# Kernel optimization log

Hardware: AMD Instinct MI355X
Metric: run time of the kernel (lower is better)

## Reference

```python
import jax, jax.numpy as jnp
import numpy as np

H = 256          # decoder_size
MAX_LENGTH = 64
VOCAB = 3


def _cell(x, h, c, w_ih, w_hh, b_ih, b_hh):
    # PyTorch LSTM cell, gate order i, f, g, o
    g = x @ w_ih.T + h @ w_hh.T + b_ih + b_hh
    i, f, gg, o = jnp.split(g, 4, axis=-1)
    c = jax.nn.sigmoid(f) * c + jax.nn.sigmoid(i) * jnp.tanh(gg)
    h = jax.nn.sigmoid(o) * jnp.tanh(c)
    return h, c


def _final_state(xs, w_ih, w_hh, b_ih, b_hh):
    # run a unidirectional LSTM over xs [T,B,D], return final (h, c)
    B = xs.shape[1]
    h0 = jnp.zeros((B, H), xs.dtype)
    c0 = jnp.zeros((B, H), xs.dtype)
    def step(carry, x):
        h, c = _cell(x, carry[0], carry[1], w_ih, w_hh, b_ih, b_hh)
        return (h, c), None
    (h, c), _ = jax.lax.scan(step, (h0, c0), xs)
    return h, c


def setup_inputs() -> dict:
    key = jax.random.key(0)
    ks = jax.random.split(key, 20)
    T, B, D = 512, 128, 1024
    s = jnp.float32(0.05)  # keep gates out of saturation
    def p(k, shape):
        return jax.random.normal(k, shape, jnp.float32) * s
    return {
        "x": jax.random.normal(ks[0], (T, B, D), jnp.float32),
        "ew_ih_f": p(ks[1], (4 * H, D)), "ew_hh_f": p(ks[2], (4 * H, H)),
        "eb_ih_f": p(ks[3], (4 * H,)),   "eb_hh_f": p(ks[4], (4 * H,)),
        "ew_ih_b": p(ks[5], (4 * H, D)), "ew_hh_b": p(ks[6], (4 * H, H)),
        "eb_ih_b": p(ks[7], (4 * H,)),   "eb_hh_b": p(ks[8], (4 * H,)),
        "dw_ih0": p(ks[9], (4 * H, H)),  "dw_hh0": p(ks[10], (4 * H, H)),
        "db_ih0": p(ks[11], (4 * H,)),   "db_hh0": p(ks[12], (4 * H,)),
        "dw_ih1": p(ks[13], (4 * H, H)), "dw_hh1": p(ks[14], (4 * H, H)),
        "db_ih1": p(ks[15], (4 * H,)),   "db_hh1": p(ks[16], (4 * H,)),
        "lw": p(ks[17], (VOCAB, H)),     "lb": p(ks[18], (VOCAB,)),
    }


def reference(x, ew_ih_f, ew_hh_f, eb_ih_f, eb_hh_f,
              ew_ih_b, ew_hh_b, eb_ih_b, eb_hh_b,
              dw_ih0, dw_hh0, db_ih0, db_hh0,
              dw_ih1, dw_hh1, db_ih1, db_hh1,
              lw, lb):
    # --- bidirectional encoder: only final hidden states are used ---
    hf, cf = _final_state(x, ew_ih_f, ew_hh_f, eb_ih_f, eb_hh_f)          # forward dir
    hb, cb = _final_state(x[::-1], ew_ih_b, ew_hh_b, eb_ih_b, eb_hh_b)    # backward dir
    # encoder h_n/c_n stacked as [fwd, bwd] -> decoder layer0, layer1 init
    B = x.shape[1]
    inp0 = jnp.zeros((B, H), x.dtype)
    def step(carry, _):
        inp, h0, c0, h1, c1 = carry
        h0, c0 = _cell(inp, h0, c0, dw_ih0, dw_hh0, db_ih0, db_hh0)
        h1, c1 = _cell(h0, h1, c1, dw_ih1, dw_hh1, db_ih1, db_hh1)
        out = h1 @ lw.T + lb  # [B, VOCAB]
        return (h1, h0, c0, h1, c1), out
    _, outs = jax.lax.scan(step, (inp0, hf, cf, hb, cb), None, length=MAX_LENGTH)
    return outs  # [MAX_LENGTH, B, VOCAB]
```

## Files before the change

### kernel.cpp

```cpp
#include <hip/hip_runtime.h>
#include <hip/hip_bf16.h>
#include <math.h>


typedef unsigned short u16;
typedef unsigned int u32;
typedef unsigned long long u64;
typedef _Float16 f16;
typedef f16 f16x8 __attribute__((ext_vector_type(8)));
typedef u16 u16x8 __attribute__((ext_vector_type(8)));
typedef u32 u32x4 __attribute__((ext_vector_type(4)));
typedef float f32x4 __attribute__((ext_vector_type(4)));

__device__ __forceinline__ u16 f2h(float f) {
  return __builtin_bit_cast(unsigned short, (f16)f);
}
__device__ __forceinline__ float h2f(u16 h) {
  return (float)__builtin_bit_cast(f16, h);
}
__device__ __forceinline__ u32 packf16(float a, float b) {
  return (u32)f2h(a) | ((u32)f2h(b) << 16);
}
__device__ __forceinline__ u64 ald64(const u64* p) {
  return __hip_atomic_load(p, __ATOMIC_RELAXED, __HIP_MEMORY_SCOPE_AGENT);
}
__device__ __forceinline__ void ast64(u64* p, u64 v) {
  __hip_atomic_store(p, v, __ATOMIC_RELAXED, __HIP_MEMORY_SCOPE_AGENT);
}

#define SENT 0xFFFFFFFFFFFFFFFFull

__global__ __launch_bounds__(256) void init_k(u32* hglob, u32* r0, u32* r1) {
  int gid = blockIdx.x * 256 + threadIdx.x;
  if (gid < 131072)       hglob[gid] = 0xFFFFFFFFu;
  else if (gid < 196608)  r0[gid - 131072] = 0xFFFFFFFFu;
  else                    r1[gid - 196608] = 0xFFFFFFFFu;
}

__global__ __launch_bounds__(256) void convert_k(
    const float* __restrict__ x,
    const float* __restrict__ wfm, const float* __restrict__ wbm,
    const float* __restrict__ bif, const float* __restrict__ bhf,
    const float* __restrict__ bib, const float* __restrict__ bhb,
    const float* __restrict__ dbi0, const float* __restrict__ dbh0,
    const float* __restrict__ dbi1, const float* __restrict__ dbh1,
    u16* __restrict__ xh, u16* __restrict__ wh,
    float* __restrict__ bias2, float* __restrict__ dbias) {
  const long NX = 67108864L, NW = 1048576L;
  long gid = (long)blockIdx.x * 256 + threadIdx.x;
  if (gid < 1024) {
    bias2[gid]        = bif[gid] + bhf[gid];
    bias2[1024 + gid] = bib[gid] + bhb[gid];
    dbias[gid]        = dbi0[gid] + dbh0[gid];
    dbias[1024 + gid] = dbi1[gid] + dbh1[gid];
  }
  long total4 = (NX + 2 * NW) >> 2;
  long stride = (long)gridDim.x * 256;
  for (long q = gid; q < total4; q += stride) {
    long i = q << 2;
    const float* src; u16* dst; long o;
    if (i < NX)            { src = x;   dst = xh;      o = i; }
    else if (i < NX + NW)  { src = wfm; dst = wh;      o = i - NX; }
    else                   { src = wbm; dst = wh + NW; o = i - NX - NW; }
    float4 v = *(const float4*)&src[o];
    dst[o + 0] = f2h(v.x); dst[o + 1] = f2h(v.y);
    dst[o + 2] = f2h(v.z); dst[o + 3] = f2h(v.w);
  }
}

__global__ __launch_bounds__(256) void convert_we3_k(
    const float* __restrict__ whf, const float* __restrict__ whb,
    u16* __restrict__ wenc3) {
  int o = blockIdx.x * 256 + threadIdx.x;
  int j = o & 7, lane = (o >> 3) & 63, ks = (o >> 9) & 7;
  int w = (o >> 12) & 3, cg = (o >> 14) & 15, d = o >> 18;
  int ri = lane & 15;
  int gcol = (ri & 3) * 256 + cg * 16 + w * 4 + (ri >> 2);
  int k = ks * 32 + (lane >> 4) * 8 + j;
  const float* wsrc = d ? whb : whf;
  wenc3[o] = f2h(wsrc[gcol * 256 + k]);
}

__global__ __launch_bounds__(256) void convert_wdec_k(
    const float* __restrict__ wi0, const float* __restrict__ wh0,
    const float* __restrict__ wi1, const float* __restrict__ wh1,
    u16* __restrict__ wdec) {
  int o = blockIdx.x * 256 + threadIdx.x;
  int j = o & 7, lane = (o >> 3) & 63, ks = (o >> 9) & 15;
  int w = (o >> 13) & 3, cg = (o >> 15) & 15, L = o >> 19;
  int ri = lane & 15;
  int row = (ri & 3) * 256 + cg * 16 + w * 4 + (ri >> 2);
  int k = ks * 32 + (lane >> 4) * 8 + j;
  const float* wi = L ? wi1 : wi0;
  const float* wh = L ? wh1 : wh0;
  float v = (k < 256) ? wi[row * 256 + k] : wh[row * 256 + k - 256];
  wdec[o] = f2h(v);
}

__global__ __launch_bounds__(256) void xproj_gemm(
    const u16* __restrict__ xh, const u16* __restrict__ wh,
    const float* __restrict__ bias2, float* __restrict__ xp) {
  __shared__ u16 Al[128][40];
  __shared__ u16 Bl[128][40];
  int bid = blockIdx.x;
  int dir = bid >> 12, rem = bid & 4095, tb = rem >> 3, nb = rem & 7;
  int tsrc = dir ? (511 - tb) : tb;
  const u16* A  = xh + (long)tsrc * (128 * 1024);
  const u16* Bw = wh + (long)dir * (1024 * 1024) + (long)nb * (128 * 1024);
  float* C = xp + ((long)(dir * 512 + tb) * 128) * 1024 + nb * 128;
  const float* bias = bias2 + dir * 1024 + nb * 128;

  int tid = threadIdx.x, lane = tid & 63, wid = tid >> 6;
  int wr = wid >> 1, wc = wid & 1;
  int srow = tid >> 1, scol = (tid & 1) * 16;
  int fr = lane & 15, ko = lane >> 4;

  f32x4 acc[4][4] = {};
  for (int k0 = 0; k0 < 1024; k0 += 32) {
    u16x8 a0 = *(const u16x8*)&A[(long)srow * 1024 + k0 + scol];
    u16x8 a1 = *(const u16x8*)&A[(long)srow * 1024 + k0 + scol + 8];
    u16x8 b0 = *(const u16x8*)&Bw[(long)srow * 1024 + k0 + scol];
    u16x8 b1 = *(const u16x8*)&Bw[(long)srow * 1024 + k0 + scol + 8];
    __syncthreads();
    *(u16x8*)&Al[srow][scol]     = a0;
    *(u16x8*)&Al[srow][scol + 8] = a1;
    *(u16x8*)&Bl[srow][scol]     = b0;
    *(u16x8*)&Bl[srow][scol + 8] = b1;
    __syncthreads();
    f16x8 af[4], bf[4];
#pragma unroll
    for (int i = 0; i < 4; ++i)
      af[i] = __builtin_bit_cast(f16x8, *(const u16x8*)&Al[wr * 64 + i * 16 + fr][ko * 8]);
#pragma unroll
    for (int jf = 0; jf < 4; ++jf)
      bf[jf] = __builtin_bit_cast(f16x8, *(const u16x8*)&Bl[wc * 64 + jf * 16 + fr][ko * 8]);
#pragma unroll
    for (int i = 0; i < 4; ++i)
#pragma unroll
      for (int jf = 0; jf < 4; ++jf)
        acc[i][jf] = __builtin_amdgcn_mfma_f32_16x16x32_f16(af[i], bf[jf], acc[i][jf], 0, 0, 0);
  }
  int fq = lane >> 4;
#pragma unroll
  for (int i = 0; i < 4; ++i)
#pragma unroll
    for (int jf = 0; jf < 4; ++jf) {
      int col = wc * 64 + jf * 16 + fr;
      float bv = bias[col];
#pragma unroll
      for (int e = 0; e < 4; ++e) {
        int row = wr * 64 + i * 16 + fq * 4 + e;
        C[(long)row * 1024 + col] = acc[i][jf][e] + bv;
      }
    }
}

__global__ __launch_bounds__(256, 1) void encoder_k(
    const u16* __restrict__ wenc3, const float* __restrict__ xp,
    u32* hglob,
    float* h0b, float* h1b, float* cfb, float* cbb) {
  int b = blockIdx.x;
  int g16 = ((b >> 7) << 3) | (b & 7);
  int cg = (b >> 3) & 15;
  int d = g16 >> 3, bg = g16 & 7;
  int tid = threadIdx.x, lane = tid & 63, w = tid >> 6;
  int brow = lane & 15, lq = lane >> 4;
  int hswz = (brow & 7) << 4;

  __shared__ __align__(16) char hlds[2][8192];
  __shared__ __align__(16) u16 hstage[16][16];

  f16x8 wfr[8];
  {
    const u16* wb = wenc3 + (((long)d * 16 + cg) * 4 + w) * 4096 + lane * 8;
#pragma unroll
    for (int ks = 0; ks < 8; ++ks)
      wfr[ks] = __builtin_bit_cast(f16x8, *(const u16x8*)(wb + (long)ks * 512));
  }

  float c_state = 0.f;
  long xpbase = ((long)(d * 512) * 128 + bg * 16 + brow) * 1024 + cg * 16 + w * 4 + lq;
  float xpv[4];
#pragma unroll
  for (int g = 0; g < 4; ++g) xpv[g] = xp[xpbase + g * 256];

  u64* hg = (u64*)hglob;
  long ringbase = (long)g16 * 4096;
  int gcg = tid >> 4, gbrow = tid & 15;
  int gldsbase = gbrow * 512 + gcg * 32;
  int gswz = (gbrow & 7) << 4;
  __syncthreads();

  for (int t = 0; t < 512; ++t) {
    if (t != 0) {
      const long gb = ringbase + (long)(t & 3) * 1024 + 4 * tid;
      u64 v0 = SENT, v1 = SENT, v2 = SENT, v3 = SENT;
      for (;;) {
        bool ok = true;
        if (v0 == SENT) { v0 = ald64(hg + gb + 0); ok &= (v0 != SENT); }
        if (v1 == SENT) { v1 = ald64(hg + gb + 1); ok &= (v1 != SENT); }
        if (v2 == SENT) { v2 = ald64(hg + gb + 2); ok &= (v2 != SENT); }
        if (v3 == SENT) { v3 = ald64(hg + gb + 3); ok &= (v3 != SENT); }
        if (ok) break;
      }
      if (tid < 64)
        ast64(hg + ringbase + (long)((t + 2) & 3) * 1024 + cg * 64 + tid, SENT);
      char* hwr = hlds[t & 1];
      *(u32x4*)(hwr + (gldsbase ^ gswz)) =
          (u32x4){ (u32)v0, (u32)(v0 >> 32), (u32)v1, (u32)(v1 >> 32) };
      *(u32x4*)(hwr + ((gldsbase + 16) ^ gswz)) =
          (u32x4){ (u32)v2, (u32)(v2 >> 32), (u32)v3, (u32)(v3 >> 32) };
    }
    __syncthreads();

    f32x4 acc0 = {}, acc1 = {};
    if (t != 0) {
      const char* hrd = hlds[t & 1];
#pragma unroll
      for (int ks = 0; ks < 8; ++ks) {
        f16x8 hf = *(const f16x8*)(hrd + ((brow * 512 + ks * 64 + lq * 16) ^ hswz));
        if (ks & 1) acc1 = __builtin_amdgcn_mfma_f32_16x16x32_f16(wfr[ks], hf, acc1, 0, 0, 0);
        else        acc0 = __builtin_amdgcn_mfma_f32_16x16x32_f16(wfr[ks], hf, acc0, 0, 0, 0);
      }
    }

    float iv = 1.f / (1.f + expf(-(acc0[0] + acc1[0] + xpv[0])));
    float fv = 1.f / (1.f + expf(-(acc0[1] + acc1[1] + xpv[1])));
    float gg = tanhf(acc0[2] + acc1[2] + xpv[2]);
    float ov = 1.f / (1.f + expf(-(acc0[3] + acc1[3] + xpv[3])));
    c_state = fv * c_state + iv * gg;
    float hval = ov * tanhf(c_state);

    if (t < 511) {
      hstage[brow][w * 4 + lq] = f2h(hval);
      __syncthreads();
      asm volatile("s_waitcnt vmcnt(0)" ::: "memory");
      if (tid < 64) {
        u64 v = *(const u64*)&hstage[tid >> 2][(tid & 3) * 4];
        ast64(hg + ringbase + (long)((t + 1) & 3) * 1024 + cg * 64 + tid, v);
      }
      long xb2 = xpbase + (long)(t + 1) * 131072;
#pragma unroll
      for (int g = 0; g < 4; ++g) xpv[g] = xp[xb2 + g * 256];
    } else {
      int rowg = bg * 16 + brow, colg = cg * 16 + w * 4 + lq;
      (d ? h1b : h0b)[32768 + rowg * 256 + colg] = hval;
      (d ? cbb : cfb)[rowg * 256 + colg] = c_state;
    }
  }
}

__global__ __launch_bounds__(256, 1) void decoder_k(
    const u16* __restrict__ wdec, const float* __restrict__ dbias,
    const float* __restrict__ h0b, const float* __restrict__ h1b,
    const float* __restrict__ cfb, const float* __restrict__ cbb,
    u32* r0, u32* r1, float* __restrict__ hist) {
  int b = blockIdx.x;
  int bg = b & 7, cg = b >> 3;
  int tid = threadIdx.x, lane = tid & 63, w = tid >> 6;
  int brow = lane & 15, lq = lane >> 4;
  int hswz = (brow & 7) << 4;
  int col = cg * 16 + w * 4 + lq;

  __shared__ __align__(16) char hA[8192];
  __shared__ __align__(16) char hB[8192];
  __shared__ __align__(16) u16 hstage[16][16];

  f16x8 w0[16], w1[16];
  {
    const u16* p0 = wdec + ((long)(cg * 4 + w)) * 8192 + lane * 8;
    const u16* p1 = wdec + ((long)((16 + cg) * 4 + w)) * 8192 + lane * 8;
#pragma unroll
    for (int ks = 0; ks < 16; ++ks) {
      w0[ks] = __builtin_bit_cast(f16x8, *(const u16x8*)(p0 + (long)ks * 512));
      w1[ks] = __builtin_bit_cast(f16x8, *(const u16x8*)(p1 + (long)ks * 512));
    }
  }
  float b0[4], b1[4];
#pragma unroll
  for (int g = 0; g < 4; ++g) {
    b0[g] = dbias[g * 256 + col];
    b1[g] = dbias[1024 + g * 256 + col];
  }
  float c0 = cfb[(bg * 16 + brow) * 256 + col];
  float c1 = cbb[(bg * 16 + brow) * 256 + col];

  int gbrow = tid & 15, gcg = tid >> 4;
  int gldsbase = gbrow * 512 + gcg * 32;
  int gswz = (gbrow & 7) << 4;
  {
    const float* sA = h0b + 32768 + (bg * 16 + gbrow) * 256 + gcg * 16;
    const float* sB = h1b + 32768 + (bg * 16 + gbrow) * 256 + gcg * 16;
    u32 wa[8], wb[8];
#pragma unroll
    for (int i = 0; i < 8; ++i) {
      wa[i] = packf16(sA[2 * i], sA[2 * i + 1]);
      wb[i] = packf16(sB[2 * i], sB[2 * i + 1]);
    }
    *(u32x4*)(hA + (gldsbase ^ gswz))        = (u32x4){wa[0], wa[1], wa[2], wa[3]};
    *(u32x4*)(hA + ((gldsbase + 16) ^ gswz)) = (u32x4){wa[4], wa[5], wa[6], wa[7]};
    *(u32x4*)(hB + (gldsbase ^ gswz))        = (u32x4){wb[0], wb[1], wb[2], wb[3]};
    *(u32x4*)(hB + ((gldsbase + 16) ^ gswz)) = (u32x4){wb[4], wb[5], wb[6], wb[7]};
  }
  __syncthreads();

  u64* g0 = (u64*)r0;
  u64* g1 = (u64*)r1;
  long ring = (long)bg * 4096;

  for (int t = 0; t < 64; ++t) {
    f32x4 a0 = {}, a1 = {};
    if (t > 0) {
#pragma unroll
      for (int ks = 0; ks < 8; ++ks) {
        f16x8 hf = *(const f16x8*)(hB + ((brow * 512 + ks * 64 + lq * 16) ^ hswz));
        if (ks & 1) a1 = __builtin_amdgcn_mfma_f32_16x16x32_f16(w0[ks], hf, a1, 0, 0, 0);
        else        a0 = __builtin_amdgcn_mfma_f32_16x16x32_f16(w0[ks], hf, a0, 0, 0, 0);
      }
    }
#pragma unroll
    for (int ks = 0; ks < 8; ++ks) {
      f16x8 hf = *(const f16x8*)(hA + ((brow * 512 + ks * 64 + lq * 16) ^ hswz));
      if (ks & 1) a1 = __builtin_amdgcn_mfma_f32_16x16x32_f16(w0[8 + ks], hf, a1, 0, 0, 0);
      else        a0 = __builtin_amdgcn_mfma_f32_16x16x32_f16(w0[8 + ks], hf, a0, 0, 0, 0);
    }
    {
      float iv = 1.f / (1.f + expf(-(a0[0] + a1[0] + b0[0])));
      float fv = 1.f / (1.f + expf(-(a0[1] + a1[1] + b0[1])));
      float gg = tanhf(a0[2] + a1[2] + b0[2]);
      float ov = 1.f / (1.f + expf(-(a0[3] + a1[3] + b0[3])));
      c0 = fv * c0 + iv * gg;
      float h0v = ov * tanhf(c0);
      hstage[brow][w * 4 + lq] = f2h(h0v);
    }
    __syncthreads();
    if (tid < 64)
      ast64(g0 + ring + (long)((t + 2) & 3) * 1024 + cg * 64 + tid, SENT);
    asm volatile("s_waitcnt vmcnt(0)" ::: "memory");
    if (tid < 64) {
      u64 v = *(const u64*)&hstage[tid >> 2][(tid & 3) * 4];
      ast64(g0 + ring + (long)(t & 3) * 1024 + cg * 64 + tid, v);
    }
    {
      const long gb = ring + (long)(t & 3) * 1024 + 4 * tid;
      u64 v0 = SENT, v1 = SENT, v2 = SENT, v3 = SENT;
      for (;;) {
        bool ok = true;
        if (v0 == SENT) { v0 = ald64(g0 + gb + 0); ok &= (v0 != SENT); }
        if (v1 == SENT) { v1 = ald64(g0 + gb + 1); ok &= (v1 != SENT); }
        if (v2 == SENT) { v2 = ald64(g0 + gb + 2); ok &= (v2 != SENT); }
        if (v3 == SENT) { v3 = ald64(g0 + gb + 3); ok &= (v3 != SENT); }
        if (ok) break;
      }
      *(u32x4*)(hA + (gldsbase ^ gswz)) =
          (u32x4){ (u32)v0, (u32)(v0 >> 32), (u32)v1, (u32)(v1 >> 32) };
      *(u32x4*)(hA + ((gldsbase + 16) ^ gswz)) =
          (u32x4){ (u32)v2, (u32)(v2 >> 32), (u32)v3, (u32)(v3 >> 32) };
    }
    __syncthreads();

    a0 = (f32x4){}; a1 = (f32x4){};
#pragma unroll
    for (int ks = 0; ks < 8; ++ks) {
      f16x8 hf = *(const f16x8*)(hA + ((brow * 512 + ks * 64 + lq * 16) ^ hswz));
      if (ks & 1) a1 = __builtin_amdgcn_mfma_f32_16x16x32_f16(w1[ks], hf, a1, 0, 0, 0);
      else        a0 = __builtin_amdgcn_mfma_f32_16x16x32_f16(w1[ks], hf, a0, 0, 0, 0);
    }
#pragma unroll
    for (int ks = 0; ks < 8; ++ks) {
      f16x8 hf = *(const f16x8*)(hB + ((brow * 512 + ks * 64 + lq * 16) ^ hswz));
      if (ks & 1) a1 = __builtin_amdgcn_mfma_f32_16x16x32_f16(w1[8 + ks], hf, a1, 0, 0, 0);
      else        a0 = __builtin_amdgcn_mfma_f32_16x16x32_f16(w1[8 + ks], hf, a0, 0, 0, 0);
    }
    {
      float iv = 1.f / (1.f + expf(-(a0[0] + a1[0] + b1[0])));
      float fv = 1.f / (1.f + expf(-(a0[1] + a1[1] + b1[1])));
      float gg = tanhf(a0[2] + a1[2] + b1[2]);
      float ov = 1.f / (1.f + expf(-(a0[3] + a1[3] + b1[3])));
      c1 = fv * c1 + iv * gg;
      float h1v = ov * tanhf(c1);
      hstage[brow][w * 4 + lq] = f2h(h1v);
    }
    __syncthreads();
    if (tid < 64) {
      u64 v = *(const u64*)&hstage[tid >> 2][(tid & 3) * 4];
      float4 hv4 = { h2f((u16)v), h2f((u16)(v >> 16)),
                     h2f((u16)(v >> 32)), h2f((u16)(v >> 48)) };
      *(float4*)&hist[((long)t * 128 + bg * 16 + (tid >> 2)) * 256 + cg * 16 + (tid & 3) * 4] = hv4;
    }
    if (t < 63) {
      if (tid < 64)
        ast64(g1 + ring + (long)((t + 2) & 3) * 1024 + cg * 64 + tid, SENT);
      asm volatile("s_waitcnt vmcnt(0)" ::: "memory");
      if (tid < 64) {
        u64 v = *(const u64*)&hstage[tid >> 2][(tid & 3) * 4];
        ast64(g1 + ring + (long)(t & 3) * 1024 + cg * 64 + tid, v);
      }
      const long gb = ring + (long)(t & 3) * 1024 + 4 * tid;
      u64 v0 = SENT, v1 = SENT, v2 = SENT, v3 = SENT;
      for (;;) {
        bool ok = true;
        if (v0 == SENT) { v0 = ald64(g1 + gb + 0); ok &= (v0 != SENT); }
        if (v1 == SENT) { v1 = ald64(g1 + gb + 1); ok &= (v1 != SENT); }
        if (v2 == SENT) { v2 = ald64(g1 + gb + 2); ok &= (v2 != SENT); }
        if (v3 == SENT) { v3 = ald64(g1 + gb + 3); ok &= (v3 != SENT); }
        if (ok) break;
      }
      *(u32x4*)(hB + (gldsbase ^ gswz)) =
          (u32x4){ (u32)v0, (u32)(v0 >> 32), (u32)v1, (u32)(v1 >> 32) };
      *(u32x4*)(hB + ((gldsbase + 16) ^ gswz)) =
          (u32x4){ (u32)v2, (u32)(v2 >> 32), (u32)v3, (u32)(v3 >> 32) };
    }
    __syncthreads();
  }
}

__global__ __launch_bounds__(256) void logits_k(
    const float* __restrict__ hist, const float* __restrict__ lw,
    const float* __restrict__ lb, float* __restrict__ out) {
  int widx = threadIdx.x >> 6, lane = threadIdx.x & 63;
  int row = blockIdx.x * 4 + widx;
  const float* h = hist + (long)row * 256;
  float4 hv = *(const float4*)&h[lane * 4];
  float s[3];
#pragma unroll
  for (int v = 0; v < 3; ++v) {
    float4 wv = *(const float4*)&lw[v * 256 + lane * 4];
    float p = hv.x * wv.x + hv.y * wv.y + hv.z * wv.z + hv.w * wv.w;
#pragma unroll
    for (int o = 32; o > 0; o >>= 1) p += __shfl_xor(p, o, 64);
    s[v] = p;
  }
  if (lane == 0) {
    out[row * 3 + 0] = s[0] + lb[0];
    out[row * 3 + 1] = s[1] + lb[1];
    out[row * 3 + 2] = s[2] + lb[2];
  }
}

extern "C" void kernel_launch(void* const* d_in, const int* in_sizes, int n_in,
                              void* d_out, int out_size, void* d_ws, size_t ws_size,
                              hipStream_t stream) {
  const float* x     = (const float*)d_in[0];
  const float* ewihf = (const float*)d_in[1];
  const float* ewhhf = (const float*)d_in[2];
  const float* ebihf = (const float*)d_in[3];
  const float* ebhhf = (const float*)d_in[4];
  const float* ewihb = (const float*)d_in[5];
  const float* ewhhb = (const float*)d_in[6];
  const float* ebihb = (const float*)d_in[7];
  const float* ebhhb = (const float*)d_in[8];
  const float* dwih0 = (const float*)d_in[9];
  const float* dwhh0 = (const float*)d_in[10];
  const float* dbih0 = (const float*)d_in[11];
  const float* dbhh0 = (const float*)d_in[12];
  const float* dwih1 = (const float*)d_in[13];
  const float* dwhh1 = (const float*)d_in[14];
  const float* dbih1 = (const float*)d_in[15];
  const float* dbhh1 = (const float*)d_in[16];
  const float* lw    = (const float*)d_in[17];
  const float* lb    = (const float*)d_in[18];
  float* out = (float*)d_out;
  (void)in_sizes; (void)n_in; (void)out_size; (void)ws_size;

  char* wsb = (char*)d_ws;
  size_t off = 0;
  auto take = [&](size_t bytes) -> char* {
    char* p = wsb + off;
    off = (off + bytes + 255) & ~(size_t)255;
    return p;
  };
  u16*   xh    = (u16*)take(67108864ull * 2);
  u16*   whx   = (u16*)take(2097152ull * 2);
  float* xp    = (float*)take(134217728ull * 4);
  u16*   wenc3 = (u16*)take(524288ull * 2);
  u16*   wdec  = (u16*)take(1048576ull * 2);
  float* bias2 = (float*)take(2048 * 4);
  float* dbias = (float*)take(2048 * 4);
  u32*   hglob = (u32*)take(131072ull * 4);
  u32*   r0    = (u32*)take(65536ull * 4);
  u32*   r1    = (u32*)take(65536ull * 4);
  float* h0b   = (float*)take(65536 * 4);
  float* h1b   = (float*)take(65536 * 4);
  float* cfb   = (float*)take(32768 * 4);
  float* cbb   = (float*)take(32768 * 4);
  float* hist  = (float*)take(2097152 * 4);

  init_k<<<1024, 256, 0, stream>>>(hglob, r0, r1);
  convert_k<<<2048, 256, 0, stream>>>(x, ewihf, ewihb, ebihf, ebhhf, ebihb, ebhhb,
                                      dbih0, dbhh0, dbih1, dbhh1, xh, whx, bias2, dbias);
  convert_we3_k<<<2048, 256, 0, stream>>>(ewhhf, ewhhb, wenc3);
  convert_wdec_k<<<4096, 256, 0, stream>>>(dwih0, dwhh0, dwih1, dwhh1, wdec);
  xproj_gemm<<<8192, 256, 0, stream>>>(xh, whx, bias2, xp);
  encoder_k<<<256, 256, 0, stream>>>(wenc3, xp, hglob, h0b, h1b, cfb, cbb);
  decoder_k<<<128, 256, 0, stream>>>(wdec, dbias, h0b, h1b, cfb, cbb, r0, r1, hist);
  logits_k<<<2048, 256, 0, stream>>>(hist, lw, lb, out);
}
```

Before: 2.092 ms.

## Fuse input-projection GEMM with encoder recurrence using per-timestep completion flags

Merges the x-projection GEMM and the encoder LSTM recurrence into one persistent launch. GEMM blocks are reordered so they finish timestep by timestep, store results atomically and bump a per-timestep counter. The encoder blocks come last in the grid and spin on that counter before reading each step's projection. The aim is to overlap the sequential encoder with the tail of the GEMM and save a kernel boundary. In exchange, the encoder can only start once the GEMM blocks ahead of it have been dispatched, the fused kernel carries the register usage of both branches, and it adds spin-wait traffic.

```diff
diff --git a/kernel.cpp b/kernel.cpp
--- a/kernel.cpp
+++ b/kernel.cpp
@@ -27,14 +27,21 @@
 __device__ __forceinline__ void ast64(u64* p, u64 v) {
   __hip_atomic_store(p, v, __ATOMIC_RELAXED, __HIP_MEMORY_SCOPE_AGENT);
 }
+__device__ __forceinline__ float aldf(const float* p) {
+  return __hip_atomic_load(p, __ATOMIC_RELAXED, __HIP_MEMORY_SCOPE_AGENT);
+}
+__device__ __forceinline__ void astf(float* p, float v) {
+  __hip_atomic_store(p, v, __ATOMIC_RELAXED, __HIP_MEMORY_SCOPE_AGENT);
+}
 
 #define SENT 0xFFFFFFFFFFFFFFFFull
 
-__global__ __launch_bounds__(256) void init_k(u32* hglob, u32* r0, u32* r1) {
+__global__ __launch_bounds__(256) void init_k(u32* hglob, u32* r0, u32* r1, int* xdone) {
   int gid = blockIdx.x * 256 + threadIdx.x;
   if (gid < 131072)       hglob[gid] = 0xFFFFFFFFu;
   else if (gid < 196608)  r0[gid - 131072] = 0xFFFFFFFFu;
   else                    r1[gid - 196608] = 0xFFFFFFFFu;
+  if (gid < 1024) xdone[gid] = 0;
 }
 
 __global__ __launch_bounds__(256) void convert_k(
@@ -97,78 +104,87 @@
   wdec[o] = f2h(v);
 }
 
-__global__ __launch_bounds__(256) void xproj_gemm(
+__global__ __launch_bounds__(256) void fused_k(
     const u16* __restrict__ xh, const u16* __restrict__ wh,
-    const float* __restrict__ bias2, float* __restrict__ xp) {
-  __shared__ u16 Al[128][40];
-  __shared__ u16 Bl[128][40];
+    const float* __restrict__ bias2, float* xp, int* xdone,
+    const u16* __restrict__ wenc3, u32* hglob,
+    float* h0b, float* h1b, float* cfb, float* cbb) {
+  __shared__ __align__(16) char smem[20992];
   int bid = blockIdx.x;
-  int dir = bid >> 12, rem = bid & 4095, tb = rem >> 3, nb = rem & 7;
-  int tsrc = dir ? (511 - tb) : tb;
-  const u16* A  = xh + (long)tsrc * (128 * 1024);
-  const u16* Bw = wh + (long)dir * (1024 * 1024) + (long)nb * (128 * 1024);
-  float* C = xp + ((long)(dir * 512 + tb) * 128) * 1024 + nb * 128;
-  const float* bias = bias2 + dir * 1024 + nb * 128;
-
-  int tid = threadIdx.x, lane = tid & 63, wid = tid >> 6;
-  int wr = wid >> 1, wc = wid & 1;
-  int srow = tid >> 1, scol = (tid & 1) * 16;
-  int fr = lane & 15, ko = lane >> 4;
-
-  f32x4 acc[4][4] = {};
-  for (int k0 = 0; k0 < 1024; k0 += 32) {
-    u16x8 a0 = *(const u16x8*)&A[(long)srow * 1024 + k0 + scol];
-    u16x8 a1 = *(const u16x8*)&A[(long)srow * 1024 + k0 + scol + 8];
-    u16x8 b0 = *(const u16x8*)&Bw[(long)srow * 1024 + k0 + scol];
-    u16x8 b1 = *(const u16x8*)&Bw[(long)srow * 1024 + k0 + scol + 8];
+  int tid = threadIdx.x;
+
+  if (bid < 8192) {
+    u16 (*Al)[40] = (u16(*)[40])smem;
+    u16 (*Bl)[40] = (u16(*)[40])(smem + 10240);
+    int tb = bid >> 4, dir = (bid >> 3) & 1, nb = bid & 7;
+    int tsrc = dir ? (511 - tb) : tb;
+    const u16* A  = xh + (long)tsrc * (128 * 1024);
+    const u16* Bw = wh + (long)dir * (1024 * 1024) + (long)nb * (128 * 1024);
+    float* C = xp + ((long)(dir * 512 + tb) * 128) * 1024 + nb * 128;
+    const float* bias = bias2 + dir * 1024 + nb * 128;
+
+    int lane = tid & 63, wid = tid >> 6;
+    int wr = wid >> 1, wc = wid & 1;
+    int srow = tid >> 1, scol = (tid & 1) * 16;
+    int fr = lane & 15, ko = lane >> 4;
+
+    f32x4 acc[4][4] = {};
+    for (int k0 = 0; k0 < 1024; k0 += 32) {
+      u16x8 a0 = *(const u16x8*)&A[(long)srow * 1024 + k0 + scol];
+      u16x8 a1 = *(const u16x8*)&A[(long)srow * 1024 + k0 + scol + 8];
+      u16x8 b0 = *(const u16x8*)&Bw[(long)srow * 1024 + k0 + scol];
+      u16x8 b1 = *(const u16x8*)&Bw[(long)srow * 1024 + k0 + scol + 8];
+      __syncthreads();
+      *(u16x8*)&Al[srow][scol]     = a0;
+      *(u16x8*)&Al[srow][scol + 8] = a1;
+      *(u16x8*)&Bl[srow][scol]     = b0;
+      *(u16x8*)&Bl[srow][scol + 8] = b1;
+      __syncthreads();
+      f16x8 af[4], bf[4];
+#pragma unroll
+      for (int i = 0; i < 4; ++i)
+        af[i] = __builtin_bit_cast(f16x8, *(const u16x8*)&Al[wr * 64 + i * 16 + fr][ko * 8]);
+#pragma unroll
+      for (int jf = 0; jf < 4; ++jf)
+        bf[jf] = __builtin_bit_cast(f16x8, *(const u16x8*)&Bl[wc * 64 + jf * 16 + fr][ko * 8]);
+#pragma unroll
+      for (int i = 0; i < 4; ++i)
+#pragma unroll
+        for (int jf = 0; jf < 4; ++jf)
+          acc[i][jf] = __builtin_amdgcn_mfma_f32_16x16x32_f16(af[i], bf[jf], acc[i][jf], 0, 0, 0);
+    }
+    int fq = lane >> 4;
+#pragma unroll
+    for (int i = 0; i < 4; ++i)
+#pragma unroll
+      for (int jf = 0; jf < 4; ++jf) {
+        int col = wc * 64 + jf * 16 + fr;
+        float bv = bias[col];
+#pragma unroll
+        for (int e = 0; e < 4; ++e) {
+          int row = wr * 64 + i * 16 + fq * 4 + e;
+          astf(&C[(long)row * 1024 + col], acc[i][jf][e] + bv);
+        }
+      }
+    asm volatile("s_waitcnt vmcnt(0)" ::: "memory");
     __syncthreads();
-    *(u16x8*)&Al[srow][scol]     = a0;
-    *(u16x8*)&Al[srow][scol + 8] = a1;
-    *(u16x8*)&Bl[srow][scol]     = b0;
-    *(u16x8*)&Bl[srow][scol + 8] = b1;
-    __syncthreads();
-    f16x8 af[4], bf[4];
-#pragma unroll
-    for (int i = 0; i < 4; ++i)
-      af[i] = __builtin_bit_cast(f16x8, *(const u16x8*)&Al[wr * 64 + i * 16 + fr][ko * 8]);
-#pragma unroll
-    for (int jf = 0; jf < 4; ++jf)
-      bf[jf] = __builtin_bit_cast(f16x8, *(const u16x8*)&Bl[wc * 64 + jf * 16 + fr][ko * 8]);
-#pragma unroll
-    for (int i = 0; i < 4; ++i)
-#pragma unroll
-      for (int jf = 0; jf < 4; ++jf)
-        acc[i][jf] = __builtin_amdgcn_mfma_f32_16x16x32_f16(af[i], bf[jf], acc[i][jf], 0, 0, 0);
-  }
-  int fq = lane >> 4;
-#pragma unroll
-  for (int i = 0; i < 4; ++i)
-#pragma unroll
-    for (int jf = 0; jf < 4; ++jf) {
-      int col = wc * 64 + jf * 16 + fr;
-      float bv = bias[col];
-#pragma unroll
-      for (int e = 0; e < 4; ++e) {
-        int row = wr * 64 + i * 16 + fq * 4 + e;
-        C[(long)row * 1024 + col] = acc[i][jf][e] + bv;
-      }
-    }
-}
-
-__global__ __launch_bounds__(256, 1) void encoder_k(
-    const u16* __restrict__ wenc3, const float* __restrict__ xp,
-    u32* hglob,
-    float* h0b, float* h1b, float* cfb, float* cbb) {
-  int b = blockIdx.x;
+    if (tid == 0)
+      __hip_atomic_fetch_add(&xdone[dir * 512 + tb], 1,
+                             __ATOMIC_RELAXED, __HIP_MEMORY_SCOPE_AGENT);
+    return;
+  }
+
+  int b = bid - 8192;
+  char* hbuf0 = smem;
+  char* hbuf1 = smem + 8192;
+  u16 (*hstage)[16] = (u16(*)[16])(smem + 16384);
+
   int g16 = ((b >> 7) << 3) | (b & 7);
   int cg = (b >> 3) & 15;
   int d = g16 >> 3, bg = g16 & 7;
-  int tid = threadIdx.x, lane = tid & 63, w = tid >> 6;
+  int lane = tid & 63, w = tid >> 6;
   int brow = lane & 15, lq = lane >> 4;
   int hswz = (brow & 7) << 4;
-
-  __shared__ __align__(16) char hlds[2][8192];
-  __shared__ __align__(16) u16 hstage[16][16];
 
   f16x8 wfr[8];
   {
@@ -178,11 +194,14 @@
       wfr[ks] = __builtin_bit_cast(f16x8, *(const u16x8*)(wb + (long)ks * 512));
   }
 
+  int* myxd = xdone + d * 512;
   float c_state = 0.f;
   long xpbase = ((long)(d * 512) * 128 + bg * 16 + brow) * 1024 + cg * 16 + w * 4 + lq;
+  while (__hip_atomic_load(&myxd[0], __ATOMIC_RELAXED, __HIP_MEMORY_SCOPE_AGENT) < 8)
+    __builtin_amdgcn_s_sleep(4);
   float xpv[4];
 #pragma unroll
-  for (int g = 0; g < 4; ++g) xpv[g] = xp[xpbase + g * 256];
+  for (int g = 0; g < 4; ++g) xpv[g] = aldf(xp + xpbase + g * 256);
 
   u64* hg = (u64*)hglob;
   long ringbase = (long)g16 * 4096;
@@ -205,7 +224,7 @@
       }
       if (tid < 64)
         ast64(hg + ringbase + (long)((t + 2) & 3) * 1024 + cg * 64 + tid, SENT);
-      char* hwr = hlds[t & 1];
+      char* hwr = (t & 1) ? hbuf1 : hbuf0;
       *(u32x4*)(hwr + (gldsbase ^ gswz)) =
           (u32x4){ (u32)v0, (u32)(v0 >> 32), (u32)v1, (u32)(v1 >> 32) };
       *(u32x4*)(hwr + ((gldsbase + 16) ^ gswz)) =
@@ -215,7 +234,7 @@
 
     f32x4 acc0 = {}, acc1 = {};
     if (t != 0) {
-      const char* hrd = hlds[t & 1];
+      const char* hrd = (t & 1) ? hbuf1 : hbuf0;
 #pragma unroll
       for (int ks = 0; ks < 8; ++ks) {
         f16x8 hf = *(const f16x8*)(hrd + ((brow * 512 + ks * 64 + lq * 16) ^ hswz));
@@ -239,9 +258,11 @@
         u64 v = *(const u64*)&hstage[tid >> 2][(tid & 3) * 4];
         ast64(hg + ringbase + (long)((t + 1) & 3) * 1024 + cg * 64 + tid, v);
       }
+      while (__hip_atomic_load(&myxd[t + 1], __ATOMIC_RELAXED, __HIP_MEMORY_SCOPE_AGENT) < 8)
+        __builtin_amdgcn_s_sleep(1);
       long xb2 = xpbase + (long)(t + 1) * 131072;
 #pragma unroll
-      for (int g = 0; g < 4; ++g) xpv[g] = xp[xb2 + g * 256];
+      for (int g = 0; g < 4; ++g) xpv[g] = aldf(xp + xb2 + g * 256);
     } else {
       int rowg = bg * 16 + brow, colg = cg * 16 + w * 4 + lq;
       (d ? h1b : h0b)[32768 + rowg * 256 + colg] = hval;
@@ -480,19 +501,20 @@
   u32*   hglob = (u32*)take(131072ull * 4);
   u32*   r0    = (u32*)take(65536ull * 4);
   u32*   r1    = (u32*)take(65536ull * 4);
+  int*   xdone = (int*)take(1024 * 4);
   float* h0b   = (float*)take(65536 * 4);
   float* h1b   = (float*)take(65536 * 4);
   float* cfb   = (float*)take(32768 * 4);
   float* cbb   = (float*)take(32768 * 4);
   float* hist  = (float*)take(2097152 * 4);
 
-  init_k<<<1024, 256, 0, stream>>>(hglob, r0, r1);
+  init_k<<<1024, 256, 0, stream>>>(hglob, r0, r1, xdone);
   convert_k<<<2048, 256, 0, stream>>>(x, ewihf, ewihb, ebihf, ebhhf, ebihb, ebhhb,
                                       dbih0, dbhh0, dbih1, dbhh1, xh, whx, bias2, dbias);
   convert_we3_k<<<2048, 256, 0, stream>>>(ewhhf, ewhhb, wenc3);
   convert_wdec_k<<<4096, 256, 0, stream>>>(dwih0, dwhh0, dwih1, dwhh1, wdec);
-  xproj_gemm<<<8192, 256, 0, stream>>>(xh, whx, bias2, xp);
-  encoder_k<<<256, 256, 0, stream>>>(wenc3, xp, hglob, h0b, h1b, cfb, cbb);
+  fused_k<<<8448, 256, 0, stream>>>(xh, whx, bias2, xp, xdone, wenc3, hglob,
+                                    h0b, h1b, cfb, cbb);
   decoder_k<<<128, 256, 0, stream>>>(wdec, dbias, h0b, h1b, cfb, cbb, r0, r1, hist);
   logits_k<<<2048, 256, 0, stream>>>(hist, lw, lb, out);
 }
```

New measurement: 2.196 ms. 1.05x slower.
